# Kernel tuning notes

Measured on AMD Instinct MI355X. Metric: run time of the kernel, lower is better.

Reference implementation:

```python
import jax, jax.numpy as jnp
import numpy as np

D_MODEL = 512
NUM_HEADS = 8
D_K = D_MODEL // NUM_HEADS
WINDOW = 65
DILATION = 1
RADIUS = WINDOW // 2
B, T = 4, 2048


def setup_inputs() -> dict:
    key = jax.random.key(0)
    ks = jax.random.split(key, 5)
    s_in = 1.0 / np.sqrt(D_MODEL)
    return {
        "x": jax.random.normal(ks[0], (B, T, D_MODEL), dtype=jnp.float32),
        "Wqkv": jax.random.normal(ks[1], (3 * D_MODEL, D_MODEL), dtype=jnp.float32) * s_in,
        "bqkv": jax.random.normal(ks[2], (3 * D_MODEL,), dtype=jnp.float32) * 0.02,
        "Wout": jax.random.normal(ks[3], (D_MODEL, D_MODEL), dtype=jnp.float32) * s_in,
        "bout": jax.random.normal(ks[4], (D_MODEL,), dtype=jnp.float32) * 0.02,
    }


def reference(x, Wqkv, bqkv, Wout, bout):
    Bsz, Tlen, D = x.shape
    scale = jnp.asarray(np.sqrt(D_K), dtype=x.dtype)

    # qkv projection (torch Linear: x @ W.T + b), chunk into q,k,v
    qkv = x @ Wqkv.T + bqkv                    # (B,T,3D)
    q, k, v = jnp.split(qkv, 3, axis=-1)
    # (B,H,T,dk)
    q = q.reshape(Bsz, Tlen, NUM_HEADS, D_K).transpose(0, 2, 1, 3)
    k = k.reshape(Bsz, Tlen, NUM_HEADS, D_K).transpose(0, 2, 1, 3)
    v = v.reshape(Bsz, Tlen, NUM_HEADS, D_K).transpose(0, 2, 1, 3)

    # Local window positions per query: t + dilation*[-radius..radius],
    # masked where out of range (equivalent to the torch per-token clamp
    # left=max(0,t-r*dil), right=min(T-1,t+r*dil) with dilation=1).
    offsets = jnp.arange(-RADIUS, RADIUS + 1) * DILATION        # (W,)
    pos = jnp.arange(Tlen)[:, None] + offsets[None, :]          # (T,W)
    valid = (pos >= 0) & (pos < Tlen)                           # (T,W)
    pos_c = jnp.clip(pos, 0, Tlen - 1)

    kw = k[:, :, pos_c]                                         # (B,H,T,W,dk)
    vw = v[:, :, pos_c]                                         # (B,H,T,W,dk)

    scores = jnp.einsum("bhtd,bhtwd->bhtw", q, kw) / scale      # (B,H,T,W)
    scores = jnp.where(valid[None, None], scores, jnp.finfo(scores.dtype).min)
    weights = jax.nn.softmax(scores, axis=-1)
    ctx = jnp.einsum("bhtw,bhtwd->bhtd", weights, vw)           # (B,H,T,dk)

    out = ctx.transpose(0, 2, 1, 3).reshape(Bsz, Tlen, D)
    out = out @ Wout.T + bout                                   # (B,T,D)
    # dropout is identity in eval mode
    return out
```

## Files before the change

### kernel.cpp

```cpp
#include <hip/hip_runtime.h>
#include <stdint.h>

#define T_LEN 2048

typedef unsigned short ushort_t;
typedef short bf16x8 __attribute__((ext_vector_type(8)));
typedef float f32x4  __attribute__((ext_vector_type(4)));

__device__ __forceinline__ unsigned short f2bf(float f) {
  union { float f; unsigned int u; } v; v.f = f;
  unsigned int u = v.u;
  return (unsigned short)((u + 0x7FFFu + ((u >> 16) & 1u)) >> 16);
}

__device__ __forceinline__ void xcd_swizzle_panel(int& bx, int& by) {
  int s = blockIdx.y * gridDim.x + blockIdx.x;
  int xcd = s & 7, idx = s >> 3;
  by = xcd + 8 * (idx / gridDim.x);
  bx = idx % gridDim.x;
}

__global__ __launch_bounds__(256) void cvt_kernel(
    const float4* __restrict__ x, const float4* __restrict__ w1, const float4* __restrict__ w2,
    ushort4* __restrict__ xb, ushort4* __restrict__ w1b, ushort4* __restrict__ w2b) {
  const int NX4 = (8192 * 512) / 4;
  const int NW14 = (1536 * 512) / 4;
  const int NW24 = (512 * 512) / 4;
  int i = blockIdx.x * 256 + threadIdx.x;
  float4 v; ushort4* dst;
  if (i < NX4) { v = x[i]; dst = xb + i; }
  else if (i < NX4 + NW14) { int j = i - NX4; v = w1[j]; dst = w1b + j; }
  else { int j = i - NX4 - NW14; if (j >= NW24) return; v = w2[j]; dst = w2b + j; }
  ushort4 o; o.x = f2bf(v.x); o.y = f2bf(v.y); o.z = f2bf(v.z); o.w = f2bf(v.w);
  *dst = o;
}

__device__ __forceinline__ void stage_192(
    const ushort_t* __restrict__ A, const ushort_t* __restrict__ Bm,
    ushort_t* As, ushort_t* Bs, int bm, int bn, int K, int kt,
    int wave, int sr8, int skb) {
#pragma unroll
  for (int c = 0; c < 2; ++c) {
    int chunk = wave * 2 + c;
    int row = chunk * 8 + sr8;
    __builtin_amdgcn_global_load_lds(
        (const __attribute__((address_space(1))) unsigned int*)
            ((const char*)(A + (size_t)(bm + row) * K + kt) + skb),
        (__attribute__((address_space(3))) unsigned int*)(As + chunk * 512),
        16, 0, 0);
  }
#pragma unroll
  for (int c = 0; c < 3; ++c) {
    int chunk = wave * 3 + c;
    int row = chunk * 8 + sr8;
    __builtin_amdgcn_global_load_lds(
        (const __attribute__((address_space(1))) unsigned int*)
            ((const char*)(Bm + (size_t)(bn + row) * K + kt) + skb),
        (__attribute__((address_space(3))) unsigned int*)(Bs + chunk * 512),
        16, 0, 0);
  }
}

__global__ __launch_bounds__(512, 4) void gemm_db192(
    const ushort_t* __restrict__ A, const ushort_t* __restrict__ Bm,
    const float* __restrict__ bias, ushort_t* __restrict__ Cb, int N, int K) {
  int bx, by; xcd_swizzle_panel(bx, by);
  const int bm = by * 128, bn = bx * 192;
  __shared__ __align__(16) ushort_t As[2][128 * 64];
  __shared__ __align__(16) ushort_t Bs[2][192 * 64];
  const int tid = threadIdx.x;
  const int lane = tid & 63, wave = tid >> 6;
  const int wr = wave & 1, wc = wave >> 1;
  const int l15 = lane & 15, lg = lane >> 4;
  const int sr8 = lane >> 3;
  const int skb = ((lane & 7) ^ sr8) << 4;
  const int sxor = (l15 & 7) << 4;
  f32x4 acc[4][3] = {};

  stage_192(A, Bm, As[0], Bs[0], bm, bn, K, 0, wave, sr8, skb);

  const int NT = K >> 6;
  for (int t = 0; t < NT; ++t) {
    const int cur = t & 1;
    if (t + 1 < NT) {
      stage_192(A, Bm, As[cur ^ 1], Bs[cur ^ 1], bm, bn, K, (t + 1) << 6,
                wave, sr8, skb);
      asm volatile("s_waitcnt vmcnt(5)" ::: "memory");
    } else {
      asm volatile("s_waitcnt vmcnt(0)" ::: "memory");
    }
    __builtin_amdgcn_s_barrier();

    bf16x8 af[2][4], bfr[2][3];
#pragma unroll
    for (int kg = 0; kg < 2; ++kg) {
#pragma unroll
      for (int m = 0; m < 4; ++m) {
        int ra = wr * 64 + m * 16 + l15;
        af[kg][m] = *(const bf16x8*)((const char*)As[cur] + ra * 128 +
                                     ((kg * 64 + lg * 16) ^ sxor));
      }
#pragma unroll
      for (int n = 0; n < 3; ++n) {
        int rb = wc * 48 + n * 16 + l15;
        bfr[kg][n] = *(const bf16x8*)((const char*)Bs[cur] + rb * 128 +
                                      ((kg * 64 + lg * 16) ^ sxor));
      }
    }
    asm volatile("s_waitcnt lgkmcnt(0)" ::: "memory");
    __builtin_amdgcn_s_barrier();

    __builtin_amdgcn_s_setprio(1);
#pragma unroll
    for (int kg = 0; kg < 2; ++kg)
#pragma unroll
      for (int m = 0; m < 4; ++m)
#pragma unroll
        for (int n = 0; n < 3; ++n)
          acc[m][n] = __builtin_amdgcn_mfma_f32_16x16x32_bf16(
              af[kg][m], bfr[kg][n], acc[m][n], 0, 0, 0);
    __builtin_amdgcn_s_setprio(0);
  }

#pragma unroll
  for (int m = 0; m < 4; ++m)
#pragma unroll
    for (int n = 0; n < 3; ++n) {
      int row0 = bm + wr * 64 + m * 16 + lg * 4;
      int col = bn + wc * 48 + n * 16 + l15;
      float bb = bias[col];
#pragma unroll
      for (int j = 0; j < 4; ++j)
        Cb[(size_t)(row0 + j) * N + col] = f2bf(acc[m][n][j] + bb);
    }
}

__device__ __forceinline__ void stage_tile64(
    const ushort_t* __restrict__ A, const ushort_t* __restrict__ Bm,
    ushort_t* As, ushort_t* Bs, int bm, int bn, int K, int kt,
    int wave, int sr8, int skb) {
#pragma unroll
  for (int c = 0; c < 2; ++c) {
    int chunk = wave * 2 + c;
    int row = chunk * 8 + sr8;
    __builtin_amdgcn_global_load_lds(
        (const __attribute__((address_space(1))) unsigned int*)
            ((const char*)(A + (size_t)(bm + row) * K + kt) + skb),
        (__attribute__((address_space(3))) unsigned int*)(As + chunk * 512),
        16, 0, 0);
  }
  {
    int row = wave * 8 + sr8;
    __builtin_amdgcn_global_load_lds(
        (const __attribute__((address_space(1))) unsigned int*)
            ((const char*)(Bm + (size_t)(bn + row) * K + kt) + skb),
        (__attribute__((address_space(3))) unsigned int*)(Bs + wave * 512),
        16, 0, 0);
  }
}

__global__ __launch_bounds__(512, 4) void gemm_db64(
    const ushort_t* __restrict__ A, const ushort_t* __restrict__ Bm,
    const float* __restrict__ bias, float* __restrict__ Cf, int N, int K) {
  int bx, by; xcd_swizzle_panel(bx, by);
  const int bm = by * 128, bn = bx * 64;
  __shared__ __align__(16) ushort_t As[2][128 * 64];
  __shared__ __align__(16) ushort_t Bs[2][64 * 64];
  const int tid = threadIdx.x;
  const int lane = tid & 63, wave = tid >> 6;
  const int wr = wave >> 1, wc = wave & 1;
  const int l15 = lane & 15, lg = lane >> 4;
  const int sr8 = lane >> 3;
  const int skb = ((lane & 7) ^ sr8) << 4;
  const int sxor = (l15 & 7) << 4;
  f32x4 acc[2][2] = {};

  stage_tile64(A, Bm, As[0], Bs[0], bm, bn, K, 0, wave, sr8, skb);

  const int NT = K >> 6;
  for (int t = 0; t < NT; ++t) {
    const int cur = t & 1;
    if (t + 1 < NT) {
      stage_tile64(A, Bm, As[cur ^ 1], Bs[cur ^ 1], bm, bn, K, (t + 1) << 6,
                   wave, sr8, skb);
      asm volatile("s_waitcnt vmcnt(3)" ::: "memory");
    } else {
      asm volatile("s_waitcnt vmcnt(0)" ::: "memory");
    }
    __builtin_amdgcn_s_barrier();

    bf16x8 af[2][2], bfr[2][2];
#pragma unroll
    for (int kg = 0; kg < 2; ++kg) {
#pragma unroll
      for (int m = 0; m < 2; ++m) {
        int ra = wr * 32 + m * 16 + l15;
        af[kg][m] = *(const bf16x8*)((const char*)As[cur] + ra * 128 +
                                     ((kg * 64 + lg * 16) ^ sxor));
      }
#pragma unroll
      for (int n = 0; n < 2; ++n) {
        int rb = wc * 32 + n * 16 + l15;
        bfr[kg][n] = *(const bf16x8*)((const char*)Bs[cur] + rb * 128 +
                                      ((kg * 64 + lg * 16) ^ sxor));
      }
    }
    asm volatile("s_waitcnt lgkmcnt(0)" ::: "memory");
    __builtin_amdgcn_s_barrier();

    __builtin_amdgcn_s_setprio(1);
#pragma unroll
    for (int kg = 0; kg < 2; ++kg)
#pragma unroll
      for (int m = 0; m < 2; ++m)
#pragma unroll
        for (int n = 0; n < 2; ++n)
          acc[m][n] = __builtin_amdgcn_mfma_f32_16x16x32_bf16(
              af[kg][m], bfr[kg][n], acc[m][n], 0, 0, 0);
    __builtin_amdgcn_s_setprio(0);
  }

#pragma unroll
  for (int m = 0; m < 2; ++m)
#pragma unroll
    for (int n = 0; n < 2; ++n) {
      int row0 = bm + wr * 32 + m * 16 + lg * 4;
      int col = bn + wc * 32 + n * 16 + l15;
      float bb = bias[col];
#pragma unroll
      for (int j = 0; j < 4; ++j)
        Cf[(size_t)(row0 + j) * N + col] = acc[m][n][j] + bb;
    }
}

__global__ __launch_bounds__(256) void attn_mfma(
    const ushort_t* __restrict__ qkv, ushort_t* __restrict__ ctx) {
  const int b = blockIdx.z, h = blockIdx.y, tB = blockIdx.x * 128;
  __shared__ __align__(16) ushort_t KsPs[192 * 72];
  __shared__ __align__(16) ushort_t Vts[64][200];
  ushort_t (*Ks)[72] = (ushort_t(*)[72])KsPs;
  const int tid = threadIdx.x;
  const int wave = tid >> 6, lane = tid & 63;
  const int l15 = lane & 15, lg = lane >> 4;
  const size_t baseBT = (size_t)b * T_LEN;

  for (int idx = tid; idx < 1536; idx += 256) {
    int key = idx >> 3, d8 = (idx & 7) << 3;
    int t = tB - 32 + key;
    bf16x8 kv = {};
    if (t >= 0 && t < T_LEN)
      kv = *(const bf16x8*)(qkv + (baseBT + t) * 1536 + 512 + h * 64 + d8);
    *(bf16x8*)&Ks[key][d8] = kv;
  }
  for (int idx = tid; idx < 1536; idx += 256) {
    int d8 = (idx / 192) << 3, key = idx % 192;
    int t = tB - 32 + key;
    bf16x8 vv = {};
    if (t >= 0 && t < T_LEN)
      vv = *(const bf16x8*)(qkv + (baseBT + t) * 1536 + 1024 + h * 64 + d8);
#pragma unroll
    for (int j = 0; j < 8; ++j) Vts[d8 + j][key] = (ushort_t)vv[j];
  }
  bf16x8 qf[2][2];
#pragma unroll
  for (int m = 0; m < 2; ++m)
#pragma unroll
    for (int kg = 0; kg < 2; ++kg) {
      int tq = tB + wave * 32 + m * 16 + l15;
      qf[m][kg] = *(const bf16x8*)(qkv + (baseBT + tq) * 1536 + h * 64 + kg * 32 + lg * 8);
    }
  __syncthreads();

  f32x4 acc[2][6] = {};
#pragma unroll
  for (int n = 0; n < 6; ++n) {
    int keyr = wave * 32 + n * 16 + l15;
#pragma unroll
    for (int kg = 0; kg < 2; ++kg) {
      bf16x8 kf = *(const bf16x8*)&Ks[keyr][kg * 32 + lg * 8];
#pragma unroll
      for (int m = 0; m < 2; ++m)
        acc[m][n] = __builtin_amdgcn_mfma_f32_16x16x32_bf16(
            qf[m][kg], kf, acc[m][n], 0, 0, 0);
    }
  }
  __syncthreads();

  ushort_t* Pw = KsPs + wave * 32 * 104;
#pragma unroll
  for (int m = 0; m < 2; ++m) {
#pragma unroll
    for (int jj = 0; jj < 4; ++jj) {
      int ql = m * 16 + lg * 4 + jj;
      float sv[6]; bool ok[6];
      float mx = -1e30f;
#pragma unroll
      for (int n = 0; n < 6; ++n) {
        int kl = n * 16 + l15;
        int tk = tB + wave * 32 - 32 + kl;
        int dd = kl - ql;
        ok[n] = (dd >= 0) && (dd <= 64) && (tk >= 0) && (tk < T_LEN);
        sv[n] = ok[n] ? acc[m][n][jj] * 0.125f : -1e30f;
        mx = fmaxf(mx, sv[n]);
      }
#pragma unroll
      for (int off = 8; off; off >>= 1) mx = fmaxf(mx, __shfl_xor(mx, off));
      float es[6], sum = 0.f;
#pragma unroll
      for (int n = 0; n < 6; ++n) { es[n] = ok[n] ? __expf(sv[n] - mx) : 0.f; sum += es[n]; }
#pragma unroll
      for (int off = 8; off; off >>= 1) sum += __shfl_xor(sum, off);
      float inv = 1.0f / sum;
#pragma unroll
      for (int n = 0; n < 6; ++n)
        Pw[ql * 104 + n * 16 + l15] = f2bf(es[n] * inv);
    }
  }
  __syncthreads();

  f32x4 acc2[2][4] = {};
#pragma unroll
  for (int ks = 0; ks < 3; ++ks) {
    bf16x8 pa[2], vb[4];
#pragma unroll
    for (int m = 0; m < 2; ++m)
      pa[m] = *(const bf16x8*)&Pw[(m * 16 + l15) * 104 + ks * 32 + lg * 8];
#pragma unroll
    for (int nn = 0; nn < 4; ++nn)
      vb[nn] = *(const bf16x8*)&Vts[nn * 16 + l15][wave * 32 + ks * 32 + lg * 8];
#pragma unroll
    for (int m = 0; m < 2; ++m)
#pragma unroll
      for (int nn = 0; nn < 4; ++nn)
        acc2[m][nn] = __builtin_amdgcn_mfma_f32_16x16x32_bf16(
            pa[m], vb[nn], acc2[m][nn], 0, 0, 0);
  }
  __syncthreads();

  ushort_t (*Ct)[72] = (ushort_t(*)[72])KsPs;
#pragma unroll
  for (int m = 0; m < 2; ++m)
#pragma unroll
    for (int nn = 0; nn < 4; ++nn)
#pragma unroll
      for (int jj = 0; jj < 4; ++jj)
        Ct[wave * 32 + m * 16 + lg * 4 + jj][nn * 16 + l15] = f2bf(acc2[m][nn][jj]);
  __syncthreads();

#pragma unroll
  for (int c = 0; c < 4; ++c) {
    int e = c * 256 + tid;
    int row = e >> 3, ch = (e & 7) << 3;
    *(bf16x8*)(ctx + (baseBT + tB + row) * 512 + h * 64 + ch) =
        *(const bf16x8*)&Ct[row][ch];
  }
}

extern "C" void kernel_launch(void* const* d_in, const int* in_sizes, int n_in,
                              void* d_out, int out_size, void* d_ws, size_t ws_size,
                              hipStream_t stream) {
  const float* x = nullptr; const float* Wqkv = nullptr; const float* bqkv = nullptr;
  const float* Wout = nullptr; const float* bout = nullptr;
  for (int i = 0; i < n_in; ++i) {
    switch (in_sizes[i]) {
      case 4194304: x    = (const float*)d_in[i]; break;
      case 786432:  Wqkv = (const float*)d_in[i]; break;
      case 1536:    bqkv = (const float*)d_in[i]; break;
      case 262144:  Wout = (const float*)d_in[i]; break;
      case 512:     bout = (const float*)d_in[i]; break;
      default: break;
    }
  }
  const size_t need_ws =
      ((size_t)8192 * 1536 + (size_t)8192 * 512 * 2 +
       (size_t)1536 * 512 + (size_t)512 * 512) * 2;
  if (!x || !Wqkv || !bqkv || !Wout || !bout || ws_size < need_ws) return;
  float* out = (float*)d_out;

  ushort_t* qkvb = (ushort_t*)d_ws;
  ushort_t* ctxb = qkvb + (size_t)8192 * 1536;
  ushort_t* xb   = ctxb + (size_t)8192 * 512;
  ushort_t* w1b  = xb + (size_t)8192 * 512;
  ushort_t* w2b  = w1b + (size_t)1536 * 512;

  cvt_kernel<<<dim3(5120), dim3(256), 0, stream>>>(
      (const float4*)x, (const float4*)Wqkv, (const float4*)Wout,
      (ushort4*)xb, (ushort4*)w1b, (ushort4*)w2b);

  gemm_db192<<<dim3(8, 64), dim3(512), 0, stream>>>(
      xb, w1b, bqkv, qkvb, 1536, 512);

  attn_mfma<<<dim3(16, 8, 4), dim3(256), 0, stream>>>(qkvb, ctxb);

  gemm_db64<<<dim3(8, 64), dim3(512), 0, stream>>>(
      ctxb, w2b, bout, out, 512, 512);
}
```

Measured before the change: 53.13 us.

## Fuse fp32-to-bf16 conversion of x into QKV GEMM A-tile staging

The separate conversion of x to bf16 is dropped. The QKV GEMM now loads fp32 x directly through registers, converts it to bf16 and writes it swizzled into LDS, while B keeps using direct global-to-LDS loads. This removes a full write and re-read of the bf16 copy of x and shrinks the conversion kernel to weights only. In exchange, each of the 8 column blocks re-reads fp32 A, which is twice the bytes of bf16. The A loads also become synchronous register loads plus LDS stores, which may weaken load/compute overlap.

```diff
diff --git a/kernel.cpp b/kernel.cpp
--- a/kernel.cpp
+++ b/kernel.cpp
@@ -11,6 +11,15 @@
   union { float f; unsigned int u; } v; v.f = f;
   unsigned int u = v.u;
   return (unsigned short)((u + 0x7FFFu + ((u >> 16) & 1u)) >> 16);
+}
+__device__ __forceinline__ bf16x8 cvt8(const float4* p) {
+  float4 a = p[0], b = p[1];
+  bf16x8 r;
+  r[0] = (short)f2bf(a.x); r[1] = (short)f2bf(a.y);
+  r[2] = (short)f2bf(a.z); r[3] = (short)f2bf(a.w);
+  r[4] = (short)f2bf(b.x); r[5] = (short)f2bf(b.y);
+  r[6] = (short)f2bf(b.z); r[7] = (short)f2bf(b.w);
+  return r;
 }
 
 __device__ __forceinline__ void xcd_swizzle_panel(int& bx, int& by) {
@@ -20,49 +29,21 @@
   bx = idx % gridDim.x;
 }
 
-__global__ __launch_bounds__(256) void cvt_kernel(
-    const float4* __restrict__ x, const float4* __restrict__ w1, const float4* __restrict__ w2,
-    ushort4* __restrict__ xb, ushort4* __restrict__ w1b, ushort4* __restrict__ w2b) {
-  const int NX4 = (8192 * 512) / 4;
+__global__ __launch_bounds__(256) void cvt_w(
+    const float4* __restrict__ w1, const float4* __restrict__ w2,
+    ushort4* __restrict__ w1b, ushort4* __restrict__ w2b) {
   const int NW14 = (1536 * 512) / 4;
   const int NW24 = (512 * 512) / 4;
   int i = blockIdx.x * 256 + threadIdx.x;
   float4 v; ushort4* dst;
-  if (i < NX4) { v = x[i]; dst = xb + i; }
-  else if (i < NX4 + NW14) { int j = i - NX4; v = w1[j]; dst = w1b + j; }
-  else { int j = i - NX4 - NW14; if (j >= NW24) return; v = w2[j]; dst = w2b + j; }
+  if (i < NW14) { v = w1[i]; dst = w1b + i; }
+  else { int j = i - NW14; if (j >= NW24) return; v = w2[j]; dst = w2b + j; }
   ushort4 o; o.x = f2bf(v.x); o.y = f2bf(v.y); o.z = f2bf(v.z); o.w = f2bf(v.w);
   *dst = o;
 }
 
-__device__ __forceinline__ void stage_192(
-    const ushort_t* __restrict__ A, const ushort_t* __restrict__ Bm,
-    ushort_t* As, ushort_t* Bs, int bm, int bn, int K, int kt,
-    int wave, int sr8, int skb) {
-#pragma unroll
-  for (int c = 0; c < 2; ++c) {
-    int chunk = wave * 2 + c;
-    int row = chunk * 8 + sr8;
-    __builtin_amdgcn_global_load_lds(
-        (const __attribute__((address_space(1))) unsigned int*)
-            ((const char*)(A + (size_t)(bm + row) * K + kt) + skb),
-        (__attribute__((address_space(3))) unsigned int*)(As + chunk * 512),
-        16, 0, 0);
-  }
-#pragma unroll
-  for (int c = 0; c < 3; ++c) {
-    int chunk = wave * 3 + c;
-    int row = chunk * 8 + sr8;
-    __builtin_amdgcn_global_load_lds(
-        (const __attribute__((address_space(1))) unsigned int*)
-            ((const char*)(Bm + (size_t)(bn + row) * K + kt) + skb),
-        (__attribute__((address_space(3))) unsigned int*)(Bs + chunk * 512),
-        16, 0, 0);
-  }
-}
-
-__global__ __launch_bounds__(512, 4) void gemm_db192(
-    const ushort_t* __restrict__ A, const ushort_t* __restrict__ Bm,
+__global__ __launch_bounds__(512, 4) void gemm1_fused(
+    const float* __restrict__ Af, const ushort_t* __restrict__ Bm,
     const float* __restrict__ bias, ushort_t* __restrict__ Cb, int N, int K) {
   int bx, by; xcd_swizzle_panel(bx, by);
   const int bm = by * 128, bn = bx * 192;
@@ -75,18 +56,45 @@
   const int sr8 = lane >> 3;
   const int skb = ((lane & 7) ^ sr8) << 4;
   const int sxor = (l15 & 7) << 4;
+  const int arow = tid >> 2, aseg = tid & 3, ar7 = arow & 7;
+  const int au0 = ((aseg * 2) ^ ar7) << 4, au1 = ((aseg * 2 + 1) ^ ar7) << 4;
+  const float* asrc = Af + (size_t)(bm + arow) * K + aseg * 16;
   f32x4 acc[4][3] = {};
 
-  stage_192(A, Bm, As[0], Bs[0], bm, bn, K, 0, wave, sr8, skb);
+#define STAGE_A(buf, kt_)                                          \
+  {                                                                \
+    const float4* ap = (const float4*)(asrc + (kt_));              \
+    bf16x8 v0 = cvt8(ap);                                          \
+    bf16x8 v1 = cvt8(ap + 2);                                      \
+    char* dst = (char*)(buf) + arow * 128;                         \
+    *(bf16x8*)(dst + au0) = v0;                                    \
+    *(bf16x8*)(dst + au1) = v1;                                    \
+  }
+#define STAGE_B(buf, kt_)                                          \
+  _Pragma("unroll")                                                \
+  for (int c = 0; c < 3; ++c) {                                    \
+    int chunk = wave * 3 + c;                                      \
+    int row = chunk * 8 + sr8;                                     \
+    __builtin_amdgcn_global_load_lds(                              \
+        (const __attribute__((address_space(1))) unsigned int*)    \
+            ((const char*)(Bm + (size_t)(bn + row) * K + (kt_)) + skb), \
+        (__attribute__((address_space(3))) unsigned int*)((buf) + chunk * 512), \
+        16, 0, 0);                                                 \
+  }
+
+  STAGE_A(As[0], 0);
+  STAGE_B(Bs[0], 0);
 
   const int NT = K >> 6;
   for (int t = 0; t < NT; ++t) {
     const int cur = t & 1;
     if (t + 1 < NT) {
-      stage_192(A, Bm, As[cur ^ 1], Bs[cur ^ 1], bm, bn, K, (t + 1) << 6,
-                wave, sr8, skb);
-      asm volatile("s_waitcnt vmcnt(5)" ::: "memory");
+      STAGE_A(As[cur ^ 1], (t + 1) << 6);
+      STAGE_B(Bs[cur ^ 1], (t + 1) << 6);
+      asm volatile("s_waitcnt lgkmcnt(0)" ::: "memory");
+      asm volatile("s_waitcnt vmcnt(3)" ::: "memory");
     } else {
+      asm volatile("s_waitcnt lgkmcnt(0)" ::: "memory");
       asm volatile("s_waitcnt vmcnt(0)" ::: "memory");
     }
     __builtin_amdgcn_s_barrier();
@@ -121,6 +129,8 @@
               af[kg][m], bfr[kg][n], acc[m][n], 0, 0, 0);
     __builtin_amdgcn_s_setprio(0);
   }
+#undef STAGE_A
+#undef STAGE_B
 
 #pragma unroll
   for (int m = 0; m < 4; ++m)
@@ -372,23 +382,22 @@
     }
   }
   const size_t need_ws =
-      ((size_t)8192 * 1536 + (size_t)8192 * 512 * 2 +
+      ((size_t)8192 * 1536 + (size_t)8192 * 512 +
        (size_t)1536 * 512 + (size_t)512 * 512) * 2;
   if (!x || !Wqkv || !bqkv || !Wout || !bout || ws_size < need_ws) return;
   float* out = (float*)d_out;
 
   ushort_t* qkvb = (ushort_t*)d_ws;
   ushort_t* ctxb = qkvb + (size_t)8192 * 1536;
-  ushort_t* xb   = ctxb + (size_t)8192 * 512;
-  ushort_t* w1b  = xb + (size_t)8192 * 512;
+  ushort_t* w1b  = ctxb + (size_t)8192 * 512;
   ushort_t* w2b  = w1b + (size_t)1536 * 512;
 
-  cvt_kernel<<<dim3(5120), dim3(256), 0, stream>>>(
-      (const float4*)x, (const float4*)Wqkv, (const float4*)Wout,
-      (ushort4*)xb, (ushort4*)w1b, (ushort4*)w2b);
-
-  gemm_db192<<<dim3(8, 64), dim3(512), 0, stream>>>(
-      xb, w1b, bqkv, qkvb, 1536, 512);
+  cvt_w<<<dim3(1024), dim3(256), 0, stream>>>(
+      (const float4*)Wqkv, (const float4*)Wout,
+      (ushort4*)w1b, (ushort4*)w2b);
+
+  gemm1_fused<<<dim3(8, 64), dim3(512), 0, stream>>>(
+      x, w1b, bqkv, qkvb, 1536, 512);
 
   attn_mfma<<<dim3(16, 8, 4), dim3(256), 0, stream>>>(qkvb, ctxb);
 
```

Measured after the change: 56.46 us. 6.3% more time.
